# Kernel tuning notes

Hardware: AMD Instinct MI355X
Metric: run time of the kernel (lower is better)

Reference implementation:

```python
import jax, jax.numpy as jnp
import numpy as np


def setup_inputs() -> dict:
    key = jax.random.key(0)
    k1, k2, k3, k4 = jax.random.split(key, 4)
    B, T, IN, D = 32, 256, 64, 128
    x = jax.random.normal(k1, (B, T, IN), dtype=jnp.float32)
    h0 = jnp.zeros((B, D), dtype=jnp.float32)
    Wx = jax.random.normal(k2, (IN, D), dtype=jnp.float32) * 0.01
    Wgate = jax.random.normal(k3, (D, D), dtype=jnp.float32) * 0.01
    Wh = jax.random.normal(k4, (D, D), dtype=jnp.float32) * 0.01
    return {"x": x, "h0": h0, "Wx": Wx, "Wgate": Wgate, "Wh": Wh}


def reference(x, h0, Wx, Wgate, Wh):
    # x: (B, T, in_dim); h0: (B, dim); returns (h_final, y, hidden_grads, dh_dWh)
    def step_single(h_r, x_r):
        # per-sample gated update: h_r (dim,), x_r (in_dim,)
        pre = x_r @ Wx + h_r @ Wh
        a = jax.nn.gelu(pre, approximate=False)  # torch GELU() is the exact erf variant
        g = jax.nn.sigmoid(a @ Wgate)
        hn = g * h_r + (1.0 - g)
        return hn, hn

    # per-step, per-sample Jacobian d h_new / d h  (mirrors vmap(jacrev(..., argnums=1)))
    jac_batched = jax.vmap(jax.jacrev(step_single, argnums=0, has_aux=True))

    def body(h, x_t):  # h: (B, dim), x_t: (B, in_dim)
        jac, h_new = jac_batched(h, x_t)  # jac: (B, dim, dim)
        return h_new, (h_new, jac)

    xt = jnp.swapaxes(x, 0, 1)  # (T, B, in_dim)
    h_final, (ys, jacs) = jax.lax.scan(body, h0, xt)
    y = jnp.swapaxes(ys, 0, 1)  # (B, T, dim)

    # last-step Jacobian wrt Wh, evaluated with the post-update h (as in the torch code)
    x_last = x[:, -1, :]

    def f_wh(Wh_):
        pre = x_last @ Wx + h_final @ Wh_
        a = jax.nn.gelu(pre, approximate=False)
        g = jax.nn.sigmoid(a @ Wgate)
        return g * h_final + (1.0 - g)

    dh_dWh = jax.jacrev(f_wh)(Wh)  # (B, dim, dim, dim)
    return (h_final, y, jacs, dh_dWh)
```

## Files before the change

### kernel.cpp

```cpp
#include <hip/hip_runtime.h>


#define JACOFF 1052672L
#define DHWOFF 135270400L

typedef __attribute__((ext_vector_type(8))) short frag_ab;
typedef __attribute__((ext_vector_type(4))) float frag_cd;

__device__ __forceinline__ short f2bf(float f) {
    unsigned u = __builtin_bit_cast(unsigned, f);
    unsigned r = (u + 0x7fffu + ((u >> 16) & 1u)) >> 16;
    return (short)r;
}

__global__ __launch_bounds__(256) void prep_xw_kernel(
    const float* __restrict__ Wh, const float* __restrict__ Wg,
    const float* __restrict__ x, const float* __restrict__ Wx,
    float* __restrict__ whT, float* __restrict__ wgT, float* __restrict__ xw)
{
    int blk = blockIdx.x;
    int tid = threadIdx.x;
    if (blk < 128) {
        int idx = blk * 256 + tid;
        if (idx < 16384) {
            int k = idx >> 7, i = idx & 127;
            whT[i * 128 + k] = Wh[idx];
        } else {
            int r = idx - 16384;
            int k = r >> 7, i = r & 127;
            wgT[i * 128 + k] = Wg[r];
        }
        return;
    }
    __shared__ float xs[2][64];
    int sub = tid >> 7;
    int bt = (blk - 128) * 2 + sub;
    int i = tid & 127;
    if (i < 64) xs[sub][i] = x[bt * 64 + i];
    __syncthreads();
    float acc = 0.f;
#pragma unroll
    for (int m = 0; m < 64; ++m)
        acc += xs[sub][m] * Wx[m * 128 + i];
    xw[bt * 128 + i] = acc;
}

__global__ __launch_bounds__(512, 1) void scan_pk_kernel(
    const float* __restrict__ xw, const float* __restrict__ h0,
    const float* __restrict__ whT, const float* __restrict__ wgT,
    const float* __restrict__ Wgate, const float* __restrict__ Wh,
    float* __restrict__ out,
    short* __restrict__ Abf, float* __restrict__ wgv, float* __restrict__ wc,
    float* __restrict__ wdF, float* __restrict__ wuF, float* __restrict__ whF,
    short* __restrict__ PT)
{
    int tid = threadIdx.x;
    if (blockIdx.x >= 32) {
        int c = (blockIdx.x - 32) * 32 + (tid >> 4);
        int k0 = (tid & 15) * 8;
        int i = c >> 7, j = c & 127;
        short v[8];
#pragma unroll
        for (int m = 0; m < 8; ++m) {
            float wg = Wgate[(k0 + m) * 128 + i];
            float wh = Wh[j * 128 + k0 + m];
            v[m] = f2bf(wg * wh);
        }
        *(frag_ab*)(PT + (long)c * 128 + k0) = *(frag_ab*)v;
        return;
    }

    const int b = blockIdx.x;
    const int i = tid >> 2, qtr = tid & 3;
    __shared__ float hbuf[2][128];
    __shared__ float abuf[128];
    float wh[32], wgc[32];
    {
        const float* whr = whT + i * 128 + qtr * 32;
        const float* wgr = wgT + i * 128 + qtr * 32;
#pragma unroll
        for (int k = 0; k < 32; k += 4) {
            float4 a4 = *(const float4*)(whr + k);
            wh[k] = a4.x; wh[k + 1] = a4.y; wh[k + 2] = a4.z; wh[k + 3] = a4.w;
            float4 b4 = *(const float4*)(wgr + k);
            wgc[k] = b4.x; wgc[k + 1] = b4.y; wgc[k + 2] = b4.z; wgc[k + 3] = b4.w;
        }
    }
    if (qtr == 0) hbuf[0][i] = h0[b * 128 + i];
    __syncthreads();

    const float inv_sqrt2 = 0.70710678118654752f;
    const float inv_sqrt2pi = 0.39894228040143268f;

    float xwv = xw[(b * 256 + 0) * 128 + i];

    for (int t = 0; t < 256; ++t) {
        int p = t & 1;
        int tn = (t < 255) ? t + 1 : 255;
        float xwn = xw[(b * 256 + tn) * 128 + i];

        float s0 = 0.f, s1 = 0.f, s2 = 0.f, s3 = 0.f;
        const float* hb = &hbuf[p][qtr * 32];
#pragma unroll
        for (int k = 0; k < 32; k += 4) {
            float4 h4 = *(const float4*)(hb + k);
            s0 += h4.x * wh[k];
            s1 += h4.y * wh[k + 1];
            s2 += h4.z * wh[k + 2];
            s3 += h4.w * wh[k + 3];
        }
        float s = (s0 + s1) + (s2 + s3);
        s += __shfl_xor(s, 1);
        s += __shfl_xor(s, 2);
        float pre = xwv + s;

        float cdf = 0.5f * (1.0f + erff(pre * inv_sqrt2));
        float a = pre * cdf;
        float dval = cdf + pre * inv_sqrt2pi * expf(-0.5f * pre * pre);

        long tb = (long)(t * 32 + b) * 128 + i;
        if (qtr == 0) {
            Abf[tb] = f2bf(dval);
            abuf[i] = a;
        }
        __syncthreads();

        float r0 = 0.f, r1 = 0.f, r2 = 0.f, r3 = 0.f;
        const float* ab = &abuf[qtr * 32];
#pragma unroll
        for (int k = 0; k < 32; k += 4) {
            float4 a4 = *(const float4*)(ab + k);
            r0 += a4.x * wgc[k];
            r1 += a4.y * wgc[k + 1];
            r2 += a4.z * wgc[k + 2];
            r3 += a4.w * wgc[k + 3];
        }
        float r = (r0 + r1) + (r2 + r3);
        r += __shfl_xor(r, 1);
        r += __shfl_xor(r, 2);
        float g = 1.0f / (1.0f + expf(-r));
        float hp = hbuf[p][i];
        float c = (hp - 1.0f) * g * (1.0f - g);
        float hn = g * hp + 1.0f - g;
        if (qtr == 0) {
            hbuf[p ^ 1][i] = hn;
            wgv[tb] = g;
            wc[tb] = c;
            out[4096 + (b * 256 + t) * 128 + i] = hn;
        }
        xwv = xwn;
        __syncthreads();
    }

    float hfin = hbuf[0][i];
    if (qtr == 0) {
        out[b * 128 + i] = hfin;
        whF[b * 128 + i] = hfin;
    }

    {
        float s0 = 0.f, s1 = 0.f, s2 = 0.f, s3 = 0.f;
        const float* hb = &hbuf[0][qtr * 32];
#pragma unroll
        for (int k = 0; k < 32; k += 4) {
            float4 h4 = *(const float4*)(hb + k);
            s0 += h4.x * wh[k];
            s1 += h4.y * wh[k + 1];
            s2 += h4.z * wh[k + 2];
            s3 += h4.w * wh[k + 3];
        }
        float s = (s0 + s1) + (s2 + s3);
        s += __shfl_xor(s, 1);
        s += __shfl_xor(s, 2);
        float pre = xwv + s;
        float cdf = 0.5f * (1.0f + erff(pre * inv_sqrt2));
        float a = pre * cdf;
        float dval = cdf + pre * inv_sqrt2pi * expf(-0.5f * pre * pre);
        if (qtr == 0) {
            wdF[b * 128 + i] = dval;
            abuf[i] = a;
        }
        __syncthreads();
        float r0 = 0.f, r1 = 0.f, r2 = 0.f, r3 = 0.f;
        const float* ab = &abuf[qtr * 32];
#pragma unroll
        for (int k = 0; k < 32; k += 4) {
            float4 a4 = *(const float4*)(ab + k);
            r0 += a4.x * wgc[k];
            r1 += a4.y * wgc[k + 1];
            r2 += a4.z * wgc[k + 2];
            r3 += a4.w * wgc[k + 3];
        }
        float r = (r0 + r1) + (r2 + r3);
        r += __shfl_xor(r, 1);
        r += __shfl_xor(r, 2);
        float g = 1.0f / (1.0f + expf(-r));
        if (qtr == 0) wuF[b * 128 + i] = (hfin - 1.0f) * g * (1.0f - g);
    }
}

__global__ __launch_bounds__(256) void jacmm_dhdw_kernel(
    const short* __restrict__ Abf,
    const short* __restrict__ PT,
    const float* __restrict__ wgv,
    const float* __restrict__ wc,
    const float* __restrict__ Wgate,
    const float* __restrict__ dF, const float* __restrict__ uF, const float* __restrict__ hF,
    float* __restrict__ out)
{
    int bx = blockIdx.x;
    int tid = threadIdx.x;
    int grp = bx / 3, rem = bx % 3;

    if (rem == 2) {
        __shared__ float hs[128], dsh[128];
        int b = grp >> 7, i = grp & 127;
        if (tid < 128) {
            hs[tid] = hF[b * 128 + tid];
            dsh[tid] = dF[b * 128 + tid];
        }
        __syncthreads();
        float u = uF[b * 128 + i];
        int q0 = (tid & 31) * 4, p0 = (tid >> 5) * 16;
        float w0 = u * dsh[q0 + 0] * Wgate[(q0 + 0) * 128 + i];
        float w1 = u * dsh[q0 + 1] * Wgate[(q0 + 1) * 128 + i];
        float w2 = u * dsh[q0 + 2] * Wgate[(q0 + 2) * 128 + i];
        float w3 = u * dsh[q0 + 3] * Wgate[(q0 + 3) * 128 + i];
        float* dst = out + DHWOFF + (long)grp * 16384;
#pragma unroll
        for (int pp = 0; pp < 16; ++pp) {
            float hp = hs[p0 + pp];
            *(float4*)(dst + (p0 + pp) * 128 + q0) = make_float4(hp * w0, hp * w1, hp * w2, hp * w3);
        }
        return;
    }

    __shared__ short Atile[128 * 128];
    __shared__ short Btile[128 * 128];

    int jb = grp * 2 + rem;
    int rb = jb & 63;
    int cb = jb >> 6;

    const short* Ag = Abf + (long)rb * (128 * 128);
    const short* Bg = PT + (long)cb * (128 * 128);

#pragma unroll
    for (int e = 0; e < 8; ++e) {
        int q = e * 256 + tid;
        int r = q >> 4;
        int s = q & 15;
        int ko = s ^ (r & 15);
        const short* srcA = Ag + r * 128 + ko * 8;
        const short* srcB = Bg + r * 128 + ko * 8;
        __builtin_amdgcn_global_load_lds(
            (const __attribute__((address_space(1))) void*)srcA,
            (__attribute__((address_space(3))) void*)(Atile + q * 8), 16, 0, 0);
        __builtin_amdgcn_global_load_lds(
            (const __attribute__((address_space(1))) void*)srcB,
            (__attribute__((address_space(3))) void*)(Btile + q * 8), 16, 0, 0);
    }

    int w = tid >> 6;
    int lane = tid & 63;
    int wr = w >> 1;
    int wcol = w & 1;
    int lrow = lane & 15;
    int quad = lane >> 4;

    long rowbase = (long)rb * 128;
    float ci[4][4], gi[4][4];
#pragma unroll
    for (int p = 0; p < 4; ++p) {
        int trow0 = wr * 64 + p * 16 + quad * 4;
#pragma unroll
        for (int reg = 0; reg < 4; ++reg) {
            long row = rowbase + trow0 + reg;
            ci[p][reg] = wc[row * 128 + cb];
            gi[p][reg] = wgv[row * 128 + cb];
        }
    }
    __syncthreads();

    frag_cd acc[4][4];
#pragma unroll
    for (int p = 0; p < 4; ++p)
#pragma unroll
        for (int q = 0; q < 4; ++q) {
            acc[p][q][0] = 0.f; acc[p][q][1] = 0.f; acc[p][q][2] = 0.f; acc[p][q][3] = 0.f;
        }

#pragma unroll
    for (int kk = 0; kk < 4; ++kk) {
        int ko = kk * 4 + quad;
        frag_ab af[4], bf[4];
#pragma unroll
        for (int p = 0; p < 4; ++p) {
            int r = wr * 64 + p * 16 + lrow;
            int chunk = r * 16 + (ko ^ (r & 15));
            af[p] = *(const frag_ab*)&Atile[chunk * 8];
        }
#pragma unroll
        for (int q = 0; q < 4; ++q) {
            int n = wcol * 64 + q * 16 + lrow;
            int chunk = n * 16 + (ko ^ (n & 15));
            bf[q] = *(const frag_ab*)&Btile[chunk * 8];
        }
#pragma unroll
        for (int p = 0; p < 4; ++p)
#pragma unroll
            for (int q = 0; q < 4; ++q)
                acc[p][q] = __builtin_amdgcn_mfma_f32_16x16x32_bf16(af[p], bf[q], acc[p][q], 0, 0, 0);
    }

#pragma unroll
    for (int p = 0; p < 4; ++p) {
        int trow0 = wr * 64 + p * 16 + quad * 4;
#pragma unroll
        for (int reg = 0; reg < 4; ++reg) {
            long row = rowbase + trow0 + reg;
            float* orow = out + JACOFF + row * 16384 + (long)cb * 128;
#pragma unroll
            for (int q = 0; q < 4; ++q) {
                int tcol = wcol * 64 + q * 16 + lrow;
                float v = ci[p][reg] * acc[p][q][reg];
                if (tcol == cb) v += gi[p][reg];
                orow[tcol] = v;
            }
        }
    }
}

extern "C" void kernel_launch(void* const* d_in, const int* in_sizes, int n_in,
                              void* d_out, int out_size, void* d_ws, size_t ws_size,
                              hipStream_t stream)
{
    (void)in_sizes; (void)n_in; (void)out_size; (void)ws_size;
    const float* x     = (const float*)d_in[0];
    const float* h0    = (const float*)d_in[1];
    const float* Wx    = (const float*)d_in[2];
    const float* Wgate = (const float*)d_in[3];
    const float* Wh    = (const float*)d_in[4];
    float* out = (float*)d_out;
    float* ws  = (float*)d_ws;

    float* xw  = ws;
    float* whT = ws + 1048576;
    float* wgT = ws + 1064960;
    float* wgv = ws + 1081344;
    float* wc  = ws + 2129920;
    float* wdF = ws + 3178496;
    float* wuF = ws + 3182592;
    float* whF = ws + 3186688;
    short* Abf = (short*)(ws + 3190784);
    short* PT  = (short*)(ws + 3715072);

    prep_xw_kernel<<<4224, 256, 0, stream>>>(Wh, Wgate, x, Wx, whT, wgT, xw);
    scan_pk_kernel<<<544, 512, 0, stream>>>(xw, h0, whT, wgT, Wgate, Wh, out,
                                            Abf, wgv, wc, wdF, wuF, whF, PT);
    jacmm_dhdw_kernel<<<12288, 256, 0, stream>>>(Abf, PT, wgv, wc, Wgate, wdF, wuF, whF, out);
}
```

Baseline: 1.085 ms.

## Fuse scan and Jacobian matmul into a persistent ticketed mega-kernel with flag sync

```diff
diff --git a/kernel.cpp b/kernel.cpp
--- a/kernel.cpp
+++ b/kernel.cpp
@@ -13,14 +13,29 @@
     return (short)r;
 }
 
+__device__ __forceinline__ void st_agent(float* p, float v) {
+    __hip_atomic_store(p, v, __ATOMIC_RELAXED, __HIP_MEMORY_SCOPE_AGENT);
+}
+__device__ __forceinline__ void st_agent_s16(short* p, short v) {
+    __hip_atomic_store(p, v, __ATOMIC_RELAXED, __HIP_MEMORY_SCOPE_AGENT);
+}
+__device__ __forceinline__ void st_agent_u64(unsigned long long* p, unsigned long long v) {
+    __hip_atomic_store(p, v, __ATOMIC_RELAXED, __HIP_MEMORY_SCOPE_AGENT);
+}
+__device__ __forceinline__ int ld_agent(const int* p) {
+    return __hip_atomic_load(p, __ATOMIC_RELAXED, __HIP_MEMORY_SCOPE_AGENT);
+}
+
 __global__ __launch_bounds__(256) void prep_xw_kernel(
     const float* __restrict__ Wh, const float* __restrict__ Wg,
     const float* __restrict__ x, const float* __restrict__ Wx,
-    float* __restrict__ whT, float* __restrict__ wgT, float* __restrict__ xw)
+    float* __restrict__ whT, float* __restrict__ wgT, float* __restrict__ xw,
+    int* __restrict__ sync)
 {
     int blk = blockIdx.x;
     int tid = threadIdx.x;
     if (blk < 128) {
+        if (blk == 0 && tid < 64) sync[tid] = 0;
         int idx = blk * 256 + tid;
         if (idx < 16384) {
             int k = idx >> 7, i = idx & 127;
@@ -45,288 +60,310 @@
     xw[bt * 128 + i] = acc;
 }
 
-__global__ __launch_bounds__(512, 1) void scan_pk_kernel(
+__global__ __launch_bounds__(512, 4) void mega_kernel(
     const float* __restrict__ xw, const float* __restrict__ h0,
     const float* __restrict__ whT, const float* __restrict__ wgT,
     const float* __restrict__ Wgate, const float* __restrict__ Wh,
     float* __restrict__ out,
     short* __restrict__ Abf, float* __restrict__ wgv, float* __restrict__ wc,
     float* __restrict__ wdF, float* __restrict__ wuF, float* __restrict__ whF,
-    short* __restrict__ PT)
+    short* __restrict__ PT, int* __restrict__ sync)
 {
+    union Sh {
+        struct { short At[128 * 128]; short Bt[128 * 128]; } jac;
+        struct { float hbuf[2][128]; float abuf[128]; } scan;
+        struct { float hs[128]; float dsh[128]; } dh;
+    };
+    __shared__ Sh sh;
+    __shared__ int tkt_s;
+
     int tid = threadIdx.x;
-    if (blockIdx.x >= 32) {
-        int c = (blockIdx.x - 32) * 32 + (tid >> 4);
-        int k0 = (tid & 15) * 8;
-        int i = c >> 7, j = c & 127;
-        short v[8];
-#pragma unroll
-        for (int m = 0; m < 8; ++m) {
-            float wg = Wgate[(k0 + m) * 128 + i];
-            float wh = Wh[j * 128 + k0 + m];
-            v[m] = f2bf(wg * wh);
-        }
-        *(frag_ab*)(PT + (long)c * 128 + k0) = *(frag_ab*)v;
+    if (tid == 0) tkt_s = atomicAdd(&sync[40], 1);
+    __syncthreads();
+    const int ticket = tkt_s;
+
+    if (ticket < 32) {
+        const int b = ticket;
+        const int i = tid >> 2, qtr = tid & 3;
+        float wh[32], wgc[32];
+        {
+            const float* whr = whT + i * 128 + qtr * 32;
+            const float* wgr = wgT + i * 128 + qtr * 32;
+#pragma unroll
+            for (int k = 0; k < 32; k += 4) {
+                float4 a4 = *(const float4*)(whr + k);
+                wh[k] = a4.x; wh[k + 1] = a4.y; wh[k + 2] = a4.z; wh[k + 3] = a4.w;
+                float4 b4 = *(const float4*)(wgr + k);
+                wgc[k] = b4.x; wgc[k + 1] = b4.y; wgc[k + 2] = b4.z; wgc[k + 3] = b4.w;
+            }
+        }
+        if (qtr == 0) sh.scan.hbuf[0][i] = h0[b * 128 + i];
+        __syncthreads();
+
+        const float inv_sqrt2 = 0.70710678118654752f;
+        const float inv_sqrt2pi = 0.39894228040143268f;
+        float xwv = xw[(b * 256 + 0) * 128 + i];
+
+        for (int t = 0; t < 256; ++t) {
+            int p = t & 1;
+            int tn = (t < 255) ? t + 1 : 255;
+            float xwn = xw[(b * 256 + tn) * 128 + i];
+
+            float s0 = 0.f, s1 = 0.f, s2 = 0.f, s3 = 0.f;
+            const float* hb = &sh.scan.hbuf[p][qtr * 32];
+#pragma unroll
+            for (int k = 0; k < 32; k += 4) {
+                float4 h4 = *(const float4*)(hb + k);
+                s0 += h4.x * wh[k];
+                s1 += h4.y * wh[k + 1];
+                s2 += h4.z * wh[k + 2];
+                s3 += h4.w * wh[k + 3];
+            }
+            float s = (s0 + s1) + (s2 + s3);
+            s += __shfl_xor(s, 1);
+            s += __shfl_xor(s, 2);
+            float pre = xwv + s;
+
+            float cdf = 0.5f * (1.0f + erff(pre * inv_sqrt2));
+            float a = pre * cdf;
+            float dval = cdf + pre * inv_sqrt2pi * expf(-0.5f * pre * pre);
+
+            long tb = (long)(t * 32 + b) * 128 + i;
+            if (qtr == 0) {
+                st_agent_s16(&Abf[tb], f2bf(dval));
+                sh.scan.abuf[i] = a;
+            }
+            __syncthreads();
+
+            float r0 = 0.f, r1 = 0.f, r2 = 0.f, r3 = 0.f;
+            const float* ab = &sh.scan.abuf[qtr * 32];
+#pragma unroll
+            for (int k = 0; k < 32; k += 4) {
+                float4 a4 = *(const float4*)(ab + k);
+                r0 += a4.x * wgc[k];
+                r1 += a4.y * wgc[k + 1];
+                r2 += a4.z * wgc[k + 2];
+                r3 += a4.w * wgc[k + 3];
+            }
+            float r = (r0 + r1) + (r2 + r3);
+            r += __shfl_xor(r, 1);
+            r += __shfl_xor(r, 2);
+            float g = 1.0f / (1.0f + expf(-r));
+            float hp = sh.scan.hbuf[p][i];
+            float c = (hp - 1.0f) * g * (1.0f - g);
+            float hn = g * hp + 1.0f - g;
+            if (qtr == 0) {
+                sh.scan.hbuf[p ^ 1][i] = hn;
+                st_agent(&wgv[tb], g);
+                st_agent(&wc[tb], c);
+                out[4096 + (b * 256 + t) * 128 + i] = hn;
+            }
+            xwv = xwn;
+            __syncthreads();
+            if (tid == 0)
+                __hip_atomic_store(&sync[b], t + 1, __ATOMIC_RELAXED, __HIP_MEMORY_SCOPE_AGENT);
+        }
+
+        float hfin = sh.scan.hbuf[0][i];
+        if (qtr == 0) {
+            out[b * 128 + i] = hfin;
+            st_agent(&whF[b * 128 + i], hfin);
+        }
+        {
+            float s0 = 0.f, s1 = 0.f, s2 = 0.f, s3 = 0.f;
+            const float* hb = &sh.scan.hbuf[0][qtr * 32];
+#pragma unroll
+            for (int k = 0; k < 32; k += 4) {
+                float4 h4 = *(const float4*)(hb + k);
+                s0 += h4.x * wh[k];
+                s1 += h4.y * wh[k + 1];
+                s2 += h4.z * wh[k + 2];
+                s3 += h4.w * wh[k + 3];
+            }
+            float s = (s0 + s1) + (s2 + s3);
+            s += __shfl_xor(s, 1);
+            s += __shfl_xor(s, 2);
+            float pre = xwv + s;
+            float cdf = 0.5f * (1.0f + erff(pre * inv_sqrt2));
+            float a = pre * cdf;
+            float dval = cdf + pre * inv_sqrt2pi * expf(-0.5f * pre * pre);
+            if (qtr == 0) {
+                st_agent(&wdF[b * 128 + i], dval);
+                sh.scan.abuf[i] = a;
+            }
+            __syncthreads();
+            float r0 = 0.f, r1 = 0.f, r2 = 0.f, r3 = 0.f;
+            const float* ab = &sh.scan.abuf[qtr * 32];
+#pragma unroll
+            for (int k = 0; k < 32; k += 4) {
+                float4 a4 = *(const float4*)(ab + k);
+                r0 += a4.x * wgc[k];
+                r1 += a4.y * wgc[k + 1];
+                r2 += a4.z * wgc[k + 2];
+                r3 += a4.w * wgc[k + 3];
+            }
+            float r = (r0 + r1) + (r2 + r3);
+            r += __shfl_xor(r, 1);
+            r += __shfl_xor(r, 2);
+            float g = 1.0f / (1.0f + expf(-r));
+            if (qtr == 0) st_agent(&wuF[b * 128 + i], (hfin - 1.0f) * g * (1.0f - g));
+        }
+        __syncthreads();
+        if (tid == 0)
+            __hip_atomic_store(&sync[b], 300, __ATOMIC_RELAXED, __HIP_MEMORY_SCOPE_AGENT);
         return;
     }
 
-    const int b = blockIdx.x;
-    const int i = tid >> 2, qtr = tid & 3;
-    __shared__ float hbuf[2][128];
-    __shared__ float abuf[128];
-    float wh[32], wgc[32];
+    if (ticket < 64) {
+        int pkb = ticket - 32;
+#pragma unroll 1
+        for (int pass = 0; pass < 16; ++pass) {
+            int c = pkb * 512 + pass * 32 + (tid >> 4);
+            int k0 = (tid & 15) * 8;
+            int i = c >> 7, j = c & 127;
+            short v[8];
+#pragma unroll
+            for (int m = 0; m < 8; ++m) {
+                float wg = Wgate[(k0 + m) * 128 + i];
+                float wh = Wh[j * 128 + k0 + m];
+                v[m] = f2bf(wg * wh);
+            }
+            unsigned long long* dst = (unsigned long long*)(PT + (long)c * 128 + k0);
+            unsigned long long* sv = (unsigned long long*)v;
+            st_agent_u64(dst, sv[0]);
+            st_agent_u64(dst + 1, sv[1]);
+        }
+        __syncthreads();
+        if (tid == 0) atomicAdd(&sync[33], 1);
+        return;
+    }
+
+    if (ticket < 64 + 8192) {
+        int jb = ticket - 64;
+        int rb = jb >> 7, cb = jb & 127;
+
+        if (tid == 0) {
+            while (ld_agent(&sync[33]) < 32) __builtin_amdgcn_s_sleep(2);
+            int thr = 4 * rb + 4;
+            for (int b = 0; b < 32; ++b)
+                while (ld_agent(&sync[b]) < thr) __builtin_amdgcn_s_sleep(2);
+        }
+        __syncthreads();
+
+        const short* Ag = Abf + (long)rb * (128 * 128);
+        const short* Bg = PT + (long)cb * (128 * 128);
+#pragma unroll
+        for (int e = 0; e < 4; ++e) {
+            int q = e * 512 + tid;
+            int r = q >> 4;
+            int s = q & 15;
+            int ko = s ^ (r & 15);
+            const short* srcA = Ag + r * 128 + ko * 8;
+            const short* srcB = Bg + r * 128 + ko * 8;
+            __builtin_amdgcn_global_load_lds(
+                (const __attribute__((address_space(1))) void*)srcA,
+                (__attribute__((address_space(3))) void*)(sh.jac.At + q * 8), 16, 0, 0);
+            __builtin_amdgcn_global_load_lds(
+                (const __attribute__((address_space(1))) void*)srcB,
+                (__attribute__((address_space(3))) void*)(sh.jac.Bt + q * 8), 16, 0, 0);
+        }
+
+        int w = tid >> 6;
+        int lane = tid & 63;
+        int wr = w & 1;
+        int wcol = w >> 1;
+        int lrow = lane & 15;
+        int quad = lane >> 4;
+
+        long rowbase = (long)rb * 128;
+        float ci[4][4], gi[4][4];
+#pragma unroll
+        for (int p = 0; p < 4; ++p) {
+            int trow0 = wr * 64 + p * 16 + quad * 4;
+#pragma unroll
+            for (int reg = 0; reg < 4; ++reg) {
+                long row = rowbase + trow0 + reg;
+                ci[p][reg] = wc[row * 128 + cb];
+                gi[p][reg] = wgv[row * 128 + cb];
+            }
+        }
+        __syncthreads();
+
+        frag_cd acc[4][2];
+#pragma unroll
+        for (int p = 0; p < 4; ++p)
+#pragma unroll
+            for (int q2 = 0; q2 < 2; ++q2) {
+                acc[p][q2][0] = 0.f; acc[p][q2][1] = 0.f;
+                acc[p][q2][2] = 0.f; acc[p][q2][3] = 0.f;
+            }
+
+#pragma unroll
+        for (int kk = 0; kk < 4; ++kk) {
+            int ko = kk * 4 + quad;
+            frag_ab af[4], bf[2];
+#pragma unroll
+            for (int p = 0; p < 4; ++p) {
+                int r = wr * 64 + p * 16 + lrow;
+                int chunk = r * 16 + (ko ^ (r & 15));
+                af[p] = *(const frag_ab*)&sh.jac.At[chunk * 8];
+            }
+#pragma unroll
+            for (int q2 = 0; q2 < 2; ++q2) {
+                int n = wcol * 32 + q2 * 16 + lrow;
+                int chunk = n * 16 + (ko ^ (n & 15));
+                bf[q2] = *(const frag_ab*)&sh.jac.Bt[chunk * 8];
+            }
+#pragma unroll
+            for (int p = 0; p < 4; ++p)
+#pragma unroll
+                for (int q2 = 0; q2 < 2; ++q2)
+                    acc[p][q2] = __builtin_amdgcn_mfma_f32_16x16x32_bf16(af[p], bf[q2], acc[p][q2], 0, 0, 0);
+        }
+
+#pragma unroll
+        for (int p = 0; p < 4; ++p) {
+            int trow0 = wr * 64 + p * 16 + quad * 4;
+#pragma unroll
+            for (int reg = 0; reg < 4; ++reg) {
+                long row = rowbase + trow0 + reg;
+                float* orow = out + JACOFF + row * 16384 + (long)cb * 128;
+#pragma unroll
+                for (int q2 = 0; q2 < 2; ++q2) {
+                    int tcol = wcol * 32 + q2 * 16 + lrow;
+                    float v = ci[p][reg] * acc[p][q2][reg];
+                    if (tcol == cb) v += gi[p][reg];
+                    orow[tcol] = v;
+                }
+            }
+        }
+        return;
+    }
+
     {
-        const float* whr = whT + i * 128 + qtr * 32;
-        const float* wgr = wgT + i * 128 + qtr * 32;
-#pragma unroll
-        for (int k = 0; k < 32; k += 4) {
-            float4 a4 = *(const float4*)(whr + k);
-            wh[k] = a4.x; wh[k + 1] = a4.y; wh[k + 2] = a4.z; wh[k + 3] = a4.w;
-            float4 b4 = *(const float4*)(wgr + k);
-            wgc[k] = b4.x; wgc[k + 1] = b4.y; wgc[k + 2] = b4.z; wgc[k + 3] = b4.w;
-        }
-    }
-    if (qtr == 0) hbuf[0][i] = h0[b * 128 + i];
-    __syncthreads();
-
-    const float inv_sqrt2 = 0.70710678118654752f;
-    const float inv_sqrt2pi = 0.39894228040143268f;
-
-    float xwv = xw[(b * 256 + 0) * 128 + i];
-
-    for (int t = 0; t < 256; ++t) {
-        int p = t & 1;
-        int tn = (t < 255) ? t + 1 : 255;
-        float xwn = xw[(b * 256 + tn) * 128 + i];
-
-        float s0 = 0.f, s1 = 0.f, s2 = 0.f, s3 = 0.f;
-        const float* hb = &hbuf[p][qtr * 32];
-#pragma unroll
-        for (int k = 0; k < 32; k += 4) {
-            float4 h4 = *(const float4*)(hb + k);
-            s0 += h4.x * wh[k];
-            s1 += h4.y * wh[k + 1];
-            s2 += h4.z * wh[k + 2];
-            s3 += h4.w * wh[k + 3];
-        }
-        float s = (s0 + s1) + (s2 + s3);
-        s += __shfl_xor(s, 1);
-        s += __shfl_xor(s, 2);
-        float pre = xwv + s;
-
-        float cdf = 0.5f * (1.0f + erff(pre * inv_sqrt2));
-        float a = pre * cdf;
-        float dval = cdf + pre * inv_sqrt2pi * expf(-0.5f * pre * pre);
-
-        long tb = (long)(t * 32 + b) * 128 + i;
-        if (qtr == 0) {
-            Abf[tb] = f2bf(dval);
-            abuf[i] = a;
-        }
-        __syncthreads();
-
-        float r0 = 0.f, r1 = 0.f, r2 = 0.f, r3 = 0.f;
-        const float* ab = &abuf[qtr * 32];
-#pragma unroll
-        for (int k = 0; k < 32; k += 4) {
-            float4 a4 = *(const float4*)(ab + k);
-            r0 += a4.x * wgc[k];
-            r1 += a4.y * wgc[k + 1];
-            r2 += a4.z * wgc[k + 2];
-            r3 += a4.w * wgc[k + 3];
-        }
-        float r = (r0 + r1) + (r2 + r3);
-        r += __shfl_xor(r, 1);
-        r += __shfl_xor(r, 2);
-        float g = 1.0f / (1.0f + expf(-r));
-        float hp = hbuf[p][i];
-        float c = (hp - 1.0f) * g * (1.0f - g);
-        float hn = g * hp + 1.0f - g;
-        if (qtr == 0) {
-            hbuf[p ^ 1][i] = hn;
-            wgv[tb] = g;
-            wc[tb] = c;
-            out[4096 + (b * 256 + t) * 128 + i] = hn;
-        }
-        xwv = xwn;
-        __syncthreads();
-    }
-
-    float hfin = hbuf[0][i];
-    if (qtr == 0) {
-        out[b * 128 + i] = hfin;
-        whF[b * 128 + i] = hfin;
-    }
-
-    {
-        float s0 = 0.f, s1 = 0.f, s2 = 0.f, s3 = 0.f;
-        const float* hb = &hbuf[0][qtr * 32];
-#pragma unroll
-        for (int k = 0; k < 32; k += 4) {
-            float4 h4 = *(const float4*)(hb + k);
-            s0 += h4.x * wh[k];
-            s1 += h4.y * wh[k + 1];
-            s2 += h4.z * wh[k + 2];
-            s3 += h4.w * wh[k + 3];
-        }
-        float s = (s0 + s1) + (s2 + s3);
-        s += __shfl_xor(s, 1);
-        s += __shfl_xor(s, 2);
-        float pre = xwv + s;
-        float cdf = 0.5f * (1.0f + erff(pre * inv_sqrt2));
-        float a = pre * cdf;
-        float dval = cdf + pre * inv_sqrt2pi * expf(-0.5f * pre * pre);
-        if (qtr == 0) {
-            wdF[b * 128 + i] = dval;
-            abuf[i] = a;
-        }
-        __syncthreads();
-        float r0 = 0.f, r1 = 0.f, r2 = 0.f, r3 = 0.f;
-        const float* ab = &abuf[qtr * 32];
-#pragma unroll
-        for (int k = 0; k < 32; k += 4) {
-            float4 a4 = *(const float4*)(ab + k);
-            r0 += a4.x * wgc[k];
-            r1 += a4.y * wgc[k + 1];
-            r2 += a4.z * wgc[k + 2];
-            r3 += a4.w * wgc[k + 3];
-        }
-        float r = (r0 + r1) + (r2 + r3);
-        r += __shfl_xor(r, 1);
-        r += __shfl_xor(r, 2);
-        float g = 1.0f / (1.0f + expf(-r));
-        if (qtr == 0) wuF[b * 128 + i] = (hfin - 1.0f) * g * (1.0f - g);
-    }
-}
-
-__global__ __launch_bounds__(256) void jacmm_dhdw_kernel(
-    const short* __restrict__ Abf,
-    const short* __restrict__ PT,
-    const float* __restrict__ wgv,
-    const float* __restrict__ wc,
-    const float* __restrict__ Wgate,
-    const float* __restrict__ dF, const float* __restrict__ uF, const float* __restrict__ hF,
-    float* __restrict__ out)
-{
-    int bx = blockIdx.x;
-    int tid = threadIdx.x;
-    int grp = bx / 3, rem = bx % 3;
-
-    if (rem == 2) {
-        __shared__ float hs[128], dsh[128];
-        int b = grp >> 7, i = grp & 127;
+        int u = ticket - (64 + 8192);
+        int b = u >> 7, i = u & 127;
+        if (tid == 0) {
+            for (int bb = 0; bb < 32; ++bb)
+                while (ld_agent(&sync[bb]) < 300) __builtin_amdgcn_s_sleep(2);
+        }
+        __syncthreads();
         if (tid < 128) {
-            hs[tid] = hF[b * 128 + tid];
-            dsh[tid] = dF[b * 128 + tid];
-        }
-        __syncthreads();
-        float u = uF[b * 128 + i];
-        int q0 = (tid & 31) * 4, p0 = (tid >> 5) * 16;
-        float w0 = u * dsh[q0 + 0] * Wgate[(q0 + 0) * 128 + i];
-        float w1 = u * dsh[q0 + 1] * Wgate[(q0 + 1) * 128 + i];
-        float w2 = u * dsh[q0 + 2] * Wgate[(q0 + 2) * 128 + i];
-        float w3 = u * dsh[q0 + 3] * Wgate[(q0 + 3) * 128 + i];
-        float* dst = out + DHWOFF + (long)grp * 16384;
-#pragma unroll
-        for (int pp = 0; pp < 16; ++pp) {
-            float hp = hs[p0 + pp];
+            sh.dh.hs[tid] = whF[b * 128 + tid];
+            sh.dh.dsh[tid] = wdF[b * 128 + tid];
+        }
+        __syncthreads();
+        float uv = wuF[b * 128 + i];
+        int q0 = (tid & 31) * 4, p0 = (tid >> 5) * 8;
+        float w0 = uv * sh.dh.dsh[q0 + 0] * Wgate[(q0 + 0) * 128 + i];
+        float w1 = uv * sh.dh.dsh[q0 + 1] * Wgate[(q0 + 1) * 128 + i];
+        float w2 = uv * sh.dh.dsh[q0 + 2] * Wgate[(q0 + 2) * 128 + i];
+        float w3 = uv * sh.dh.dsh[q0 + 3] * Wgate[(q0 + 3) * 128 + i];
+        float* dst = out + DHWOFF + (long)u * 16384;
+#pragma unroll
+        for (int pp = 0; pp < 8; ++pp) {
+            float hp = sh.dh.hs[p0 + pp];
             *(float4*)(dst + (p0 + pp) * 128 + q0) = make_float4(hp * w0, hp * w1, hp * w2, hp * w3);
-        }
-        return;
-    }
-
-    __shared__ short Atile[128 * 128];
-    __shared__ short Btile[128 * 128];
-
-    int jb = grp * 2 + rem;
-    int rb = jb & 63;
-    int cb = jb >> 6;
-
-    const short* Ag = Abf + (long)rb * (128 * 128);
-    const short* Bg = PT + (long)cb * (128 * 128);
-
-#pragma unroll
-    for (int e = 0; e < 8; ++e) {
-        int q = e * 256 + tid;
-        int r = q >> 4;
-        int s = q & 15;
-        int ko = s ^ (r & 15);
-        const short* srcA = Ag + r * 128 + ko * 8;
-        const short* srcB = Bg + r * 128 + ko * 8;
-        __builtin_amdgcn_global_load_lds(
-            (const __attribute__((address_space(1))) void*)srcA,
-            (__attribute__((address_space(3))) void*)(Atile + q * 8), 16, 0, 0);
-        __builtin_amdgcn_global_load_lds(
-            (const __attribute__((address_space(1))) void*)srcB,
-            (__attribute__((address_space(3))) void*)(Btile + q * 8), 16, 0, 0);
-    }
-
-    int w = tid >> 6;
-    int lane = tid & 63;
-    int wr = w >> 1;
-    int wcol = w & 1;
-    int lrow = lane & 15;
-    int quad = lane >> 4;
-
-    long rowbase = (long)rb * 128;
-    float ci[4][4], gi[4][4];
-#pragma unroll
-    for (int p = 0; p < 4; ++p) {
-        int trow0 = wr * 64 + p * 16 + quad * 4;
-#pragma unroll
-        for (int reg = 0; reg < 4; ++reg) {
-            long row = rowbase + trow0 + reg;
-            ci[p][reg] = wc[row * 128 + cb];
-            gi[p][reg] = wgv[row * 128 + cb];
-        }
-    }
-    __syncthreads();
-
-    frag_cd acc[4][4];
-#pragma unroll
-    for (int p = 0; p < 4; ++p)
-#pragma unroll
-        for (int q = 0; q < 4; ++q) {
-            acc[p][q][0] = 0.f; acc[p][q][1] = 0.f; acc[p][q][2] = 0.f; acc[p][q][3] = 0.f;
-        }
-
-#pragma unroll
-    for (int kk = 0; kk < 4; ++kk) {
-        int ko = kk * 4 + quad;
-        frag_ab af[4], bf[4];
-#pragma unroll
-        for (int p = 0; p < 4; ++p) {
-            int r = wr * 64 + p * 16 + lrow;
-            int chunk = r * 16 + (ko ^ (r & 15));
-            af[p] = *(const frag_ab*)&Atile[chunk * 8];
-        }
-#pragma unroll
-        for (int q = 0; q < 4; ++q) {
-            int n = wcol * 64 + q * 16 + lrow;
-            int chunk = n * 16 + (ko ^ (n & 15));
-            bf[q] = *(const frag_ab*)&Btile[chunk * 8];
-        }
-#pragma unroll
-        for (int p = 0; p < 4; ++p)
-#pragma unroll
-            for (int q = 0; q < 4; ++q)
-                acc[p][q] = __builtin_amdgcn_mfma_f32_16x16x32_bf16(af[p], bf[q], acc[p][q], 0, 0, 0);
-    }
-
-#pragma unroll
-    for (int p = 0; p < 4; ++p) {
-        int trow0 = wr * 64 + p * 16 + quad * 4;
-#pragma unroll
-        for (int reg = 0; reg < 4; ++reg) {
-            long row = rowbase + trow0 + reg;
-            float* orow = out + JACOFF + row * 16384 + (long)cb * 128;
-#pragma unroll
-            for (int q = 0; q < 4; ++q) {
-                int tcol = wcol * 64 + q * 16 + lrow;
-                float v = ci[p][reg] * acc[p][q][reg];
-                if (tcol == cb) v += gi[p][reg];
-                orow[tcol] = v;
-            }
         }
     }
 }
@@ -354,9 +391,9 @@
     float* whF = ws + 3186688;
     short* Abf = (short*)(ws + 3190784);
     short* PT  = (short*)(ws + 3715072);
-
-    prep_xw_kernel<<<4224, 256, 0, stream>>>(Wh, Wgate, x, Wx, whT, wgT, xw);
-    scan_pk_kernel<<<544, 512, 0, stream>>>(xw, h0, whT, wgT, Wgate, Wh, out,
-                                            Abf, wgv, wc, wdF, wuF, whF, PT);
-    jacmm_dhdw_kernel<<<12288, 256, 0, stream>>>(Abf, PT, wgv, wc, Wgate, wdF, wuF, whF, out);
-}
+    int*   syn = (int*)(ws + 4763648);
+
+    prep_xw_kernel<<<4224, 256, 0, stream>>>(Wh, Wgate, x, Wx, whT, wgT, xw, syn);
+    mega_kernel<<<12352, 512, 0, stream>>>(xw, h0, whT, wgT, Wgate, Wh, out,
+                                           Abf, wgv, wc, wdF, wuF, whF, PT, syn);
+}
```

Result: slower. 1.516 ms (+39.7%).
